# Performance work log

Hardware: AMD Instinct MI355X
Metric: run time of the kernel (lower is better)

Reference implementation:

```python
import jax, jax.numpy as jnp
import numpy as np

B, S, N = 64, 32, 128            # batch, seq_len, padded nodes per graph
DV, DW, DH = 512, 300, 1024      # dim_v, dim_word, dim_hidden
CLS, T_CTRL, L = 1024, 12, 4     # cls_fc_dim, controller steps, stack_len
NQ, NA, NE, NATTR, M = 100, 28, 16, 1000, 6  # vocabs, edge cats, attrs, num modules
# module order: 0 NoOp, 1 Find(push), 2 Transform, 3 Filter, 4 And, 5 Describe

def _valid_mat():
    m = np.zeros((L, M), dtype=np.float32)
    for s in range(L):
        m[s, 0] = 1.0
        m[s, 1] = 1.0 if s < L - 1 else 0.0
        m[s, 2] = 1.0 if s >= 1 else 0.0
        m[s, 3] = 1.0 if s >= 1 else 0.0
        m[s, 4] = 1.0 if s >= 2 else 0.0
        m[s, 5] = 1.0 if s >= 1 else 0.0
    return jnp.asarray(m)

VALID_MAT = _valid_mat()

def setup_inputs() -> dict:
    key = jax.random.key(0)
    ks = jax.random.split(key, 24)
    nrm = lambda k, sh, sc: jax.random.normal(k, sh, jnp.float32) * sc
    inp = {}
    inp['questions'] = jax.random.randint(ks[0], (B, S), 0, NQ)
    inp['questions_len'] = jax.random.randint(ks[1], (B,), 8, S + 1)
    inp['conn'] = (jax.random.uniform(ks[2], (B, N, N)) < 0.2).astype(jnp.float32)
    inp['cat_mat'] = jax.random.randint(ks[3], (B, N, N), 0, NE)
    inp['v_idx'] = jax.random.randint(ks[4], (B, N), 0, NATTR)
    inp['attr_emb'] = nrm(ks[5], (NATTR, DV), 1.0 / np.sqrt(DV))
    inp['edge_cat_vectors'] = nrm(ks[6], (NE, DV), 1.0 / np.sqrt(DV))
    inp['enc_emb'] = nrm(ks[7], (NQ, DW), 1.0 / np.sqrt(DW))
    inp['Wx'] = nrm(ks[8], (DW, 4 * DH), 1.0 / np.sqrt(DW))
    inp['Wh'] = nrm(ks[9], (DH, 4 * DH), 1.0 / np.sqrt(DH))
    inp['b_lstm'] = jnp.zeros((4 * DH,), jnp.float32)
    inp['W_cq'] = nrm(ks[10], (2 * DH, DH), 1.0 / np.sqrt(2 * DH))
    inp['b_cq'] = jnp.zeros((DH,), jnp.float32)
    inp['W_mod'] = nrm(ks[11], (DH, M), 1.0 / np.sqrt(DH))
    inp['W_att'] = nrm(ks[12], (DH, DH), 1.0 / np.sqrt(DH))
    inp['W_q'] = nrm(ks[13], (DH, DV), np.sqrt(2.0 / DH))
    inp['b_q'] = jnp.zeros((DV,), jnp.float32)
    inp['W_find'] = nrm(ks[14], (DV, DV), 1.0 / np.sqrt(DV))
    inp['W_desc'] = nrm(ks[15], (DV, DV), 1.0 / np.sqrt(DV))
    inp['W_cls1'] = nrm(ks[16], (DV + DH, CLS), np.sqrt(2.0 / (DV + DH)))
    inp['b_cls1'] = jnp.zeros((CLS,), jnp.float32)
    inp['W_cls2'] = nrm(ks[17], (CLS, NA), np.sqrt(2.0 / CLS))
    inp['b_cls2'] = jnp.zeros((NA,), jnp.float32)
    return inp

def _read(st, p):
    return jnp.einsum('bnl,bl->bn', st, p)

def _write(st, p, a):
    pe = p[:, None, :]
    return a[:, :, None] * pe + st * (1.0 - pe)

def _ptr_fw(p):
    q = jnp.concatenate([jnp.zeros_like(p[:, :1]), p[:, :-1]], axis=1)
    return q.at[:, -1].add(p[:, -1])

def _ptr_bw(p):
    q = jnp.concatenate([p[:, 1:], jnp.zeros_like(p[:, :1])], axis=1)
    return q.at[:, 0].add(p[:, 0])

def reference(questions, questions_len, conn, cat_mat, v_idx, attr_emb,
              edge_cat_vectors, enc_emb, Wx, Wh, b_lstm, W_cq, b_cq, W_mod,
              W_att, W_q, b_q, W_find, W_desc, W_cls1, b_cls1, W_cls2, b_cls2):
    # ---- question encoder: embedding + LSTM over time-major sequence ----
    emb = enc_emb[questions].transpose(1, 0, 2)  # [S,B,DW]

    def lstm_step(carry, x):
        h, c = carry
        g = x @ Wx + h @ Wh + b_lstm
        i, f, gg, o = jnp.split(g, 4, axis=-1)
        c = jax.nn.sigmoid(f) * c + jax.nn.sigmoid(i) * jnp.tanh(gg)
        h = jax.nn.sigmoid(o) * jnp.tanh(c)
        return (h, c), h

    init = (jnp.zeros((B, DH), jnp.float32), jnp.zeros((B, DH), jnp.float32))
    _, outs = jax.lax.scan(lstm_step, init, emb)            # [S,B,DH]
    outs_b = outs.transpose(1, 0, 2)                         # [B,S,DH]
    q_hidden = outs_b[jnp.arange(B), questions_len - 1]      # last valid state

    mask = jnp.arange(S)[:, None] < questions_len[None, :]   # [S,B]
    feat = attr_emb[v_idx]                                   # [B,N,DV]
    bidx = jnp.arange(B)[:, None, None]

    att_stack = jnp.zeros((B, N, L), jnp.float32)
    stack_ptr = jnp.zeros((B, L), jnp.float32).at[:, 0].set(1.0)
    mem = jnp.zeros((B, DV), jnp.float32)
    c_ctrl = jnp.zeros((B, DH), jnp.float32)
    inv_sqrt_dv = 1.0 / np.sqrt(DV)

    for t in range(T_CTRL):
        # ---- controller step: module distribution + textual attention ----
        cq = jnp.tanh(jnp.concatenate([c_ctrl, q_hidden], axis=1) @ W_cq + b_cq)
        module_prob = jax.nn.softmax(cq @ W_mod, axis=-1)     # [B,M]
        al = jnp.einsum('sbh,bh->sb', outs, cq @ W_att)
        cv = jax.nn.softmax(jnp.where(mask, al, -1e9), axis=0)
        c_ctrl = jnp.einsum('sb,sbh->bh', cv, outs)
        c_i = jax.nn.relu(c_ctrl @ W_q + b_q)                 # [B,DV]

        # ---- validity masking of module distribution ----
        validity = jnp.round(stack_ptr @ VALID_MAT)           # [B,M]
        mp = module_prob * validity
        s = jnp.sum(mp, axis=1, keepdims=True)
        mp = mp / jnp.where(s > 0, s, 1.0)

        # ---- run every module, soft-average by module prob ----
        a_find = jax.nn.sigmoid(jnp.einsum('bnd,bd->bn', feat @ W_find, c_i) * inv_sqrt_dv)
        a_in = _read(att_stack, stack_ptr)
        # Transform: edge-category-weighted message passing on graph
        we = jax.nn.softmax(c_i @ edge_cat_vectors.T, axis=-1)   # [B,NE]
        ew = we[bidx, cat_mat] * conn                            # [B,N,N]
        a_trans = jnp.minimum(jnp.einsum('bij,bj->bi', ew, a_in), 1.0)
        p_fw = _ptr_fw(stack_ptr)
        p_bw = _ptr_bw(stack_ptr)
        a_prev = _read(att_stack, p_bw)
        pooled = jnp.einsum('bn,bnd->bd', a_in, feat) / (jnp.sum(a_in, 1, keepdims=True) + 1e-6)
        res = [
            (att_stack, stack_ptr, mem),                                  # NoOp
            (_write(att_stack, p_fw, a_find), p_fw, mem),                 # Find (push)
            (_write(att_stack, stack_ptr, a_trans), stack_ptr, mem),      # Transform
            (_write(att_stack, stack_ptr, a_in * a_find), stack_ptr, mem),# Filter
            (_write(att_stack, p_bw, jnp.minimum(a_prev, a_in)), p_bw, mem),  # And (pop)
            (att_stack, p_bw, pooled @ W_desc),                           # Describe
        ]
        att_stack = jnp.einsum('bm,mbnl->bnl', mp, jnp.stack([r[0] for r in res]))
        stack_ptr = jnp.einsum('bm,mbl->bl', mp, jnp.stack([r[1] for r in res]))
        mem = jnp.einsum('bm,mbd->bd', mp, jnp.stack([r[2] for r in res]))

    final = jnp.concatenate([mem, q_hidden], axis=1)
    h1 = jax.nn.relu(final @ W_cls1 + b_cls1)
    logits = h1 @ W_cls2 + b_cls2
    return logits
```

## Files before the change

### kernel.cpp

```cpp
#include <hip/hip_runtime.h>
#include <math.h>

#define B 64
#define S 32
#define NN 128
#define DV 512
#define DW 300
#define DH 1024
#define CLS 1024
#define T_CTRL 12
#define LL 4
#define NA 28
#define NE 16
#define MM 6

__device__ __forceinline__ float sigmoidf_(float x) { return 1.0f / (1.0f + expf(-x)); }

template<bool TRANS, class AF, class WF>
__device__ __forceinline__ void gemm_core(int kbeg, int Kc, AF loadA, WF loadW, float* part, int Cld) {
  __shared__ float Ast[2][64 * 36];
  __shared__ float Ws[2][32 * 64];
  const int tid = threadIdx.x;
  const int j0 = blockIdx.x * 64;
  const int ntiles = Kc >> 5;
  const int rg = tid & 15, cg = tid >> 4;
  float4 av[2], wv[2];

  auto fetch = [&](int kt) {
    #pragma unroll
    for (int i2 = 0; i2 < 2; ++i2) {
      int idx = tid + i2 * 256;
      av[i2] = loadA(idx >> 3, kt + (idx & 7) * 4);
    }
    #pragma unroll
    for (int i2 = 0; i2 < 2; ++i2) {
      int idx = tid + i2 * 256;
      if (!TRANS) wv[i2] = loadW(kt + (idx >> 4), j0 + (idx & 15) * 4);
      else        wv[i2] = loadW(j0 + (idx >> 3), kt + (idx & 7) * 4);
    }
  };
  auto commit = [&](int buf) {
    #pragma unroll
    for (int i2 = 0; i2 < 2; ++i2) {
      int idx = tid + i2 * 256;
      *(float4*)&Ast[buf][(idx >> 3) * 36 + (idx & 7) * 4] = av[i2];
    }
    #pragma unroll
    for (int i2 = 0; i2 < 2; ++i2) {
      int idx = tid + i2 * 256;
      if (!TRANS) {
        *(float4*)&Ws[buf][(idx >> 4) * 64 + (idx & 15) * 4] = wv[i2];
      } else {
        int jloc = idx >> 3, k4 = (idx & 7) * 4;
        Ws[buf][(k4 + 0) * 64 + jloc] = wv[i2].x;
        Ws[buf][(k4 + 1) * 64 + jloc] = wv[i2].y;
        Ws[buf][(k4 + 2) * 64 + jloc] = wv[i2].z;
        Ws[buf][(k4 + 3) * 64 + jloc] = wv[i2].w;
      }
    }
  };

  float acc[4][4] = {};
  fetch(kbeg);
  commit(0);
  __syncthreads();
  for (int i = 0; i < ntiles; ++i) {
    if (i + 1 < ntiles) fetch(kbeg + (i + 1) * 32);
    const float* As = &Ast[i & 1][0];
    const float* Wp = &Ws[i & 1][0];
    #pragma unroll
    for (int kq = 0; kq < 8; ++kq) {
      float4 a0 = *(const float4*)&As[(rg     ) * 36 + kq * 4];
      float4 a1 = *(const float4*)&As[(rg + 16) * 36 + kq * 4];
      float4 a2 = *(const float4*)&As[(rg + 32) * 36 + kq * 4];
      float4 a3 = *(const float4*)&As[(rg + 48) * 36 + kq * 4];
      float4 w0 = *(const float4*)&Wp[(kq * 4 + 0) * 64 + cg * 4];
      float4 w1 = *(const float4*)&Wp[(kq * 4 + 1) * 64 + cg * 4];
      float4 w2 = *(const float4*)&Wp[(kq * 4 + 2) * 64 + cg * 4];
      float4 w3 = *(const float4*)&Wp[(kq * 4 + 3) * 64 + cg * 4];
      #define STEP(m, AV) \
        acc[m][0]=fmaf(AV.x,w0.x,acc[m][0]); acc[m][1]=fmaf(AV.x,w0.y,acc[m][1]); \
        acc[m][2]=fmaf(AV.x,w0.z,acc[m][2]); acc[m][3]=fmaf(AV.x,w0.w,acc[m][3]); \
        acc[m][0]=fmaf(AV.y,w1.x,acc[m][0]); acc[m][1]=fmaf(AV.y,w1.y,acc[m][1]); \
        acc[m][2]=fmaf(AV.y,w1.z,acc[m][2]); acc[m][3]=fmaf(AV.y,w1.w,acc[m][3]); \
        acc[m][0]=fmaf(AV.z,w2.x,acc[m][0]); acc[m][1]=fmaf(AV.z,w2.y,acc[m][1]); \
        acc[m][2]=fmaf(AV.z,w2.z,acc[m][2]); acc[m][3]=fmaf(AV.z,w2.w,acc[m][3]); \
        acc[m][0]=fmaf(AV.w,w3.x,acc[m][0]); acc[m][1]=fmaf(AV.w,w3.y,acc[m][1]); \
        acc[m][2]=fmaf(AV.w,w3.z,acc[m][2]); acc[m][3]=fmaf(AV.w,w3.w,acc[m][3]);
      STEP(0, a0) STEP(1, a1) STEP(2, a2) STEP(3, a3)
      #undef STEP
    }
    if (i + 1 < ntiles) { __syncthreads(); commit((i + 1) & 1); __syncthreads(); }
  }
  float* op = part + (size_t)blockIdx.y * 64 * Cld + j0 + cg * 4;
  #pragma unroll
  for (int m = 0; m < 4; ++m)
    *(float4*)&op[(size_t)(rg + 16 * m) * Cld] = make_float4(acc[m][0], acc[m][1], acc[m][2], acc[m][3]);
}

__global__ void init_kernel(float* c_lstm, float* c_ctrl, float* att_stack, float* mem, float* sptr) {
  int idx = blockIdx.x * 256 + threadIdx.x;
  if (idx < B * DH) { c_lstm[idx] = 0.f; c_ctrl[idx] = 0.f; }
  if (idx < B * NN * LL) att_stack[idx] = 0.f;
  if (idx < B * DV) mem[idx] = 0.f;
  if (idx < B * LL) sptr[idx] = ((idx & (LL - 1)) == 0) ? 1.f : 0.f;
}

__global__ void embq_kernel(const int* __restrict__ questions, const float* __restrict__ enc_emb,
                            float* __restrict__ embq) {
  int row = blockIdx.x;
  int t = row >> 6, b = row & 63;
  int qid = questions[b * S + t];
  int c = threadIdx.x;
  embq[(size_t)row * 320 + c] = (c < DW) ? enc_emb[(size_t)qid * DW + c] : 0.f;
}

__global__ __launch_bounds__(256) void xgemm_kernel(const float* __restrict__ embq,
                                                    const float* __restrict__ Wx,
                                                    float* __restrict__ X) {
  auto Al = [&](int r, int k) -> float4 {
    return *(const float4*)&embq[(size_t)(blockIdx.y * 64 + r) * 320 + k];
  };
  auto Wl = [&](int k, int j) -> float4 {
    if (k < 300) return *(const float4*)&Wx[(size_t)k * 4096 + j];
    return make_float4(0.f, 0.f, 0.f, 0.f);
  };
  gemm_core<false>(0, 320, Al, Wl, X, 4096);
}

__global__ __launch_bounds__(256) void lstm_gemm_kernel(const float* __restrict__ h_prev,
                                                        const float* __restrict__ Wh,
                                                        float* __restrict__ part) {
  auto Al = [&](int r, int k) -> float4 { return *(const float4*)&h_prev[(size_t)r * 1024 + k]; };
  auto Wl = [&](int k, int j) -> float4 { return *(const float4*)&Wh[(size_t)k * 4096 + j]; };
  gemm_core<false>(blockIdx.y * 256, 256, Al, Wl, part, 4096);
}

__global__ __launch_bounds__(256) void lstm_gate_kernel(const float* __restrict__ part, int SK,
                                                        const float* __restrict__ X, int t,
                                                        const float* __restrict__ b_lstm,
                                                        float* __restrict__ h_out, float* __restrict__ c_st) {
  int idx = blockIdx.x * 256 + threadIdx.x;
  int b = idx >> 10, j = idx & 1023;
  const float* xr = X + ((size_t)t * 64 + b) * 4096;
  float gi = xr[j], gf = xr[1024 + j], gg = xr[2048 + j], go = xr[3072 + j];
  const float* pb = part + (size_t)b * 4096;
  for (int c = 0; c < SK; ++c) {
    const float* p = pb + (size_t)c * 262144;
    gi += p[j]; gf += p[1024 + j]; gg += p[2048 + j]; go += p[3072 + j];
  }
  gi += b_lstm[j]; gf += b_lstm[1024 + j]; gg += b_lstm[2048 + j]; go += b_lstm[3072 + j];
  float c = sigmoidf_(gf) * c_st[idx] + sigmoidf_(gi) * tanhf(gg);
  h_out[idx] = sigmoidf_(go) * tanhf(c);
  c_st[idx] = c;
}

__global__ __launch_bounds__(256) void c1_kernel(const float* __restrict__ c_ctrl,
                                                 const float* __restrict__ outs, const int* __restrict__ qlen,
                                                 const float* __restrict__ W_cq, float* __restrict__ partA,
                                                 const float* __restrict__ partE, const float* __restrict__ mp,
                                                 float* __restrict__ mem, int do_epi) {
  if (blockIdx.x == 16) {
    if (!do_epi) return;
    int t0 = blockIdx.y * 256 + threadIdx.x;
    #pragma unroll
    for (int i = 0; i < 4; ++i) {
      int f4 = t0 + i * 2048;
      int b = f4 >> 7, j = (f4 & 127) * 4;
      const float* m = &mp[b * 6];
      float s04 = m[0] + m[1] + m[2] + m[3] + m[4];
      float4 s = make_float4(0.f, 0.f, 0.f, 0.f);
      for (int c = 0; c < 8; ++c) {
        float4 v = *(const float4*)&partE[(size_t)c * 32768 + b * 512 + j];
        s.x += v.x; s.y += v.y; s.z += v.z; s.w += v.w;
      }
      float4 o = *(const float4*)&mem[b * 512 + j];
      o.x = s04 * o.x + m[5] * s.x; o.y = s04 * o.y + m[5] * s.y;
      o.z = s04 * o.z + m[5] * s.z; o.w = s04 * o.w + m[5] * s.w;
      *(float4*)&mem[b * 512 + j] = o;
    }
    return;
  }
  auto Al = [&](int r, int k) -> float4 {
    if (k < 1024) return *(const float4*)&c_ctrl[r * 1024 + k];
    int tq = qlen[r] - 1;
    return *(const float4*)&outs[(size_t)tq * 65536 + r * 1024 + (k - 1024)];
  };
  auto Wl = [&](int k, int j) -> float4 { return *(const float4*)&W_cq[(size_t)k * 1024 + j]; };
  gemm_core<false>(blockIdx.y * 256, 256, Al, Wl, partA, 1024);
}

__global__ __launch_bounds__(256) void c2_kernel(const float* __restrict__ partA,
                                                 const float* __restrict__ b_cq,
                                                 const float* __restrict__ W_att,
                                                 const float* __restrict__ W_mod,
                                                 float* __restrict__ partB) {
  auto Al = [&](int r, int k) -> float4 {
    float4 s = *(const float4*)&b_cq[k];
    for (int c = 0; c < 8; ++c) {
      float4 v = *(const float4*)&partA[(size_t)c * 65536 + r * 1024 + k];
      s.x += v.x; s.y += v.y; s.z += v.z; s.w += v.w;
    }
    return make_float4(tanhf(s.x), tanhf(s.y), tanhf(s.z), tanhf(s.w));
  };
  auto Wl = [&](int k, int j) -> float4 {
    if (j < 1024) return *(const float4*)&W_att[(size_t)k * 1024 + j];
    float v[4];
    #pragma unroll
    for (int i = 0; i < 4; ++i) {
      int jj = j + i;
      v[i] = (jj < 1030) ? W_mod[(size_t)k * 6 + (jj - 1024)] : 0.f;
    }
    return make_float4(v[0], v[1], v[2], v[3]);
  };
  gemm_core<false>(blockIdx.y * 64, 64, Al, Wl, partB, 1088);
}

__global__ __launch_bounds__(256) void attn_kernel(const float* __restrict__ partB,
                                                   const float* __restrict__ outs,
                                                   const int* __restrict__ qlen,
                                                   float* __restrict__ c_ctrl) {
  int b = blockIdx.x >> 2, hq = blockIdx.x & 3;
  int tid = threadIdx.x;
  __shared__ float aw[DH];
  __shared__ float alv[S];
  __shared__ float cvs[S];
  {
    int c4 = tid * 4;
    float4 s = make_float4(0.f, 0.f, 0.f, 0.f);
    for (int c = 0; c < 16; ++c) {
      float4 v = *(const float4*)&partB[(size_t)c * 69632 + b * 1088 + c4];
      s.x += v.x; s.y += v.y; s.z += v.z; s.w += v.w;
    }
    *(float4*)&aw[c4] = s;
  }
  __syncthreads();
  {
    int wv = tid >> 6, lane = tid & 63;
    #pragma unroll
    for (int u = 0; u < 4; ++u) {
      int s2 = wv * 4 + u;
      const float4* orow = (const float4*)&outs[(size_t)s2 * 65536 + b * 1024];
      float pr = 0.f;
      #pragma unroll
      for (int q = 0; q < 4; ++q) {
        float4 f = orow[lane + 64 * q];
        float4 w = *(const float4*)&aw[(lane + 64 * q) * 4];
        pr += f.x * w.x + f.y * w.y + f.z * w.z + f.w * w.w;
      }
      #pragma unroll
      for (int off = 32; off > 0; off >>= 1) pr += __shfl_xor(pr, off);
      if (lane == 0) alv[s2] = pr;
    }
  }
  __syncthreads();
  if (tid < 64) {
    int len = qlen[b];
    float v = (tid < S && tid < len) ? alv[tid] : -1e9f;
    float mx = v;
    #pragma unroll
    for (int off = 32; off > 0; off >>= 1) mx = fmaxf(mx, __shfl_xor(mx, off));
    float e = (tid < S && tid < len) ? expf(v - mx) : 0.f;
    float sm = e;
    #pragma unroll
    for (int off = 32; off > 0; off >>= 1) sm += __shfl_xor(sm, off);
    if (tid < S) cvs[tid] = e / sm;
  }
  __syncthreads();
  {
    int h = hq * 256 + tid;
    float a = 0.f;
    #pragma unroll 8
    for (int s2 = 0; s2 < S; ++s2)
      a = fmaf(cvs[s2], outs[(size_t)s2 * 65536 + b * 1024 + h], a);
    c_ctrl[b * 1024 + h] = a;
  }
}

__global__ __launch_bounds__(256) void c4_kernel(const float* __restrict__ c_ctrl,
                                                 const float* __restrict__ W_q,
                                                 float* __restrict__ partC) {
  auto Al = [&](int r, int k) -> float4 { return *(const float4*)&c_ctrl[r * 1024 + k]; };
  auto Wl = [&](int k, int j) -> float4 { return *(const float4*)&W_q[(size_t)k * 512 + j]; };
  gemm_core<false>(blockIdx.y * 64, 64, Al, Wl, partC, 512);
}

__global__ __launch_bounds__(256) void c5_kernel(const float* __restrict__ partC,
                                                 const float* __restrict__ b_q,
                                                 const float* __restrict__ W_find,
                                                 const float* __restrict__ edge_cat,
                                                 float* __restrict__ partD) {
  auto Al = [&](int r, int k) -> float4 {
    float4 s = *(const float4*)&b_q[k];
    for (int c = 0; c < 16; ++c) {
      float4 v = *(const float4*)&partC[(size_t)c * 32768 + r * 512 + k];
      s.x += v.x; s.y += v.y; s.z += v.z; s.w += v.w;
    }
    return make_float4(fmaxf(s.x, 0.f), fmaxf(s.y, 0.f), fmaxf(s.z, 0.f), fmaxf(s.w, 0.f));
  };
  auto Wl = [&](int j, int k) -> float4 {
    if (j < 512) return *(const float4*)&W_find[(size_t)j * 512 + k];
    if (j < 528) return *(const float4*)&edge_cat[(size_t)(j - 512) * 512 + k];
    return make_float4(0.f, 0.f, 0.f, 0.f);
  };
  gemm_core<true>(blockIdx.y * 64, 64, Al, Wl, partD, 576);
}

__global__ __launch_bounds__(256) void prep_kernel(const float* __restrict__ partD,
                                                   const float* __restrict__ partB,
                                                   const float* __restrict__ sptr_in,
                                                   const float* __restrict__ att_stack,
                                                   float* __restrict__ uwe, float* __restrict__ we,
                                                   float* __restrict__ mp, float* __restrict__ spv,
                                                   float* __restrict__ ain, float* __restrict__ aw4,
                                                   float* __restrict__ asum) {
  int b = blockIdx.x, tid = threadIdx.x;
  __shared__ float lds[64];
  for (int col = tid; col < 528; col += 256) {
    float s = 0.f;
    for (int c = 0; c < 8; ++c) s += partD[(size_t)c * 36864 + b * 576 + col];
    uwe[b * 528 + col] = s;
    if (col >= 512) lds[col - 512] = s;
  }
  if (tid < MM) {
    float s = 0.f;
    for (int c = 0; c < 16; ++c) s += partB[(size_t)c * 69632 + b * 1088 + 1024 + tid];
    lds[16 + tid] = s;
  }
  __syncthreads();
  if (tid == 0) {
    float mx = lds[0];
    for (int e = 1; e < NE; ++e) mx = fmaxf(mx, lds[e]);
    float sm = 0.f, ex[NE];
    for (int e = 0; e < NE; ++e) { ex[e] = expf(lds[e] - mx); sm += ex[e]; }
    for (int e = 0; e < NE; ++e) we[b * NE + e] = ex[e] / sm;
    float mx2 = lds[16];
    for (int m = 1; m < MM; ++m) mx2 = fmaxf(mx2, lds[16 + m]);
    float e6[MM], sm2 = 0.f;
    for (int m = 0; m < MM; ++m) { e6[m] = expf(lds[16 + m] - mx2); sm2 += e6[m]; }
    float p0 = sptr_in[b * 4 + 0], p1 = sptr_in[b * 4 + 1];
    float p2 = sptr_in[b * 4 + 2], p3 = sptr_in[b * 4 + 3];
    float sp[12];
    sp[0] = p0; sp[1] = p1; sp[2] = p2; sp[3] = p3;
    sp[4] = 0.f;      sp[5] = p0; sp[6] = p1; sp[7] = p2 + p3;
    sp[8] = p0 + p1;  sp[9] = p2; sp[10] = p3; sp[11] = 0.f;
    for (int i = 0; i < 12; ++i) { spv[b * 12 + i] = sp[i]; lds[22 + i] = sp[i]; }
    float val[MM];
    val[0] = rintf(p0 + p1 + p2 + p3);
    val[1] = rintf(p0 + p1 + p2);
    val[2] = rintf(p1 + p2 + p3);
    val[3] = val[2];
    val[4] = rintf(p2 + p3);
    val[5] = val[2];
    float mpv[MM], ssum = 0.f;
    #pragma unroll
    for (int m = 0; m < MM; ++m) { mpv[m] = (e6[m] / sm2) * val[m]; ssum += mpv[m]; }
    float inv = (ssum > 0.f) ? 1.f / ssum : 1.f;
    #pragma unroll
    for (int m = 0; m < MM; ++m) mp[b * MM + m] = mpv[m] * inv;
  }
  __syncthreads();
  if (tid < 128) {
    float4 st = *(const float4*)&att_stack[(b * NN + tid) * LL];
    float ainv = st.x * lds[22] + st.y * lds[23] + st.z * lds[24] + st.w * lds[25];
    float ap   = st.x * lds[30] + st.y * lds[31] + st.z * lds[32] + st.w * lds[33];
    ain[b * NN + tid] = ainv;
    aw4[b * NN + tid] = fminf(ap, ainv);
    float t2 = ainv;
    #pragma unroll
    for (int off = 32; off > 0; off >>= 1) t2 += __shfl_xor(t2, off);
    if ((tid & 63) == 0) lds[40 + (tid >> 6)] = t2;
  }
  __syncthreads();
  if (tid == 0) asum[b] = lds[40] + lds[41] + 1e-6f;
}

__global__ __launch_bounds__(256) void stackf_kernel(const int* __restrict__ v_idx,
                                                     const float* __restrict__ attr_emb,
                                                     const float* __restrict__ uwe,
                                                     const float* __restrict__ we,
                                                     const int* __restrict__ cat_mat,
                                                     const float* __restrict__ conn,
                                                     const float* __restrict__ ain,
                                                     const float* __restrict__ asum,
                                                     float* __restrict__ afind,
                                                     float* __restrict__ atr,
                                                     float* __restrict__ pooled) {
  int job = blockIdx.x, tid = threadIdx.x;
  __shared__ float lds[192];
  if (job < 2048) {
    int gw = job * 4 + (tid >> 6);
    int b = gw >> 7, n = gw & 127, lane = tid & 63;
    int vid = v_idx[b * NN + n];
    const float4* fp = (const float4*)&attr_emb[(size_t)vid * DV];
    const float4* up = (const float4*)&uwe[(size_t)b * 528];
    float pr = 0.f;
    #pragma unroll
    for (int q = 0; q < 2; ++q) {
      float4 f = fp[lane + 64 * q], u = up[lane + 64 * q];
      pr += f.x * u.x + f.y * u.y + f.z * u.z + f.w * u.w;
    }
    #pragma unroll
    for (int off = 32; off > 0; off >>= 1) pr += __shfl_xor(pr, off);
    if (lane == 0) afind[b * NN + n] = sigmoidf_(pr * 0.04419417382415922f);
  } else if (job < 2560) {
    int j2 = job - 2048;
    int b = j2 >> 3, ig = j2 & 7;
    if (tid < 128) lds[tid] = ain[b * NN + tid];
    else if (tid < 144) lds[tid] = we[b * NE + tid - 128];
    __syncthreads();
    int i = ig * 16 + (tid >> 4);
    const int* crow = &cat_mat[((size_t)b * NN + i) * NN];
    const float* nrow = &conn[((size_t)b * NN + i) * NN];
    float a = 0.f;
    #pragma unroll
    for (int q = 0; q < 8; ++q) {
      int j = (tid & 15) + 16 * q;
      a = fmaf(lds[128 + crow[j]] * nrow[j], lds[j], a);
    }
    a += __shfl_xor(a, 1); a += __shfl_xor(a, 2); a += __shfl_xor(a, 4); a += __shfl_xor(a, 8);
    if ((tid & 15) == 0) atr[b * NN + i] = fminf(a, 1.f);
  } else {
    int j3 = job - 2560;
    int b = j3 >> 1, d = (j3 & 1) * 256 + tid;
    int* vidL = (int*)&lds[128];
    if (tid < 128) { lds[tid] = ain[b * NN + tid]; vidL[tid] = v_idx[b * NN + tid]; }
    __syncthreads();
    float a = 0.f;
    #pragma unroll 4
    for (int n = 0; n < NN; ++n)
      a = fmaf(lds[n], attr_emb[(size_t)vidL[n] * DV + d], a);
    pooled[b * DV + d] = a / asum[b];
  }
}

__global__ __launch_bounds__(256) void c7u_kernel(const float* __restrict__ pooled,
                                                  const float* __restrict__ W_desc,
                                                  float* __restrict__ partE,
                                                  const float* __restrict__ spv,
                                                  const float* __restrict__ mp,
                                                  const float* __restrict__ afind,
                                                  const float* __restrict__ ain,
                                                  const float* __restrict__ atr,
                                                  const float* __restrict__ aw4,
                                                  float* __restrict__ att_stack,
                                                  float* __restrict__ sptr) {
  int tid = threadIdx.x;
  if (blockIdx.y < 8) {
    auto Al = [&](int r, int k) -> float4 { return *(const float4*)&pooled[r * 512 + k]; };
    auto Wl = [&](int k, int j) -> float4 { return *(const float4*)&W_desc[(size_t)k * 512 + j]; };
    gemm_core<false>(blockIdx.y * 64, 64, Al, Wl, partE, 512);
    return;
  }
  int b = (blockIdx.y - 8) * 8 + blockIdx.x;
  __shared__ float sp[12], smp[MM];
  if (tid < 12) sp[tid] = spv[b * 12 + tid];
  else if (tid < 12 + MM) smp[tid - 12] = mp[b * MM + (tid - 12)];
  __syncthreads();
  #pragma unroll
  for (int i = 0; i < 2; ++i) {
    int e = tid + i * 256;
    int n = e >> 2, l = e & 3;
    float st = att_stack[(b * NN + n) * LL + l];
    float keep = smp[0] + smp[5] + smp[1] * (1.f - sp[4 + l]) + (smp[2] + smp[3]) * (1.f - sp[l])
               + smp[4] * (1.f - sp[8 + l]);
    float add = sp[4 + l] * smp[1] * afind[b * NN + n]
              + sp[l] * (smp[2] * atr[b * NN + n] + smp[3] * ain[b * NN + n] * afind[b * NN + n])
              + sp[8 + l] * smp[4] * aw4[b * NN + n];
    att_stack[(b * NN + n) * LL + l] = keep * st + add;
  }
  if (tid < LL)
    sptr[b * LL + tid] = (smp[0] + smp[2] + smp[3]) * sp[tid] + smp[1] * sp[4 + tid]
                       + (smp[4] + smp[5]) * sp[8 + tid];
}

__global__ __launch_bounds__(256) void cl1_kernel(const float* __restrict__ partE,
                                                  const float* __restrict__ mp,
                                                  const float* __restrict__ mem,
                                                  const float* __restrict__ outs,
                                                  const int* __restrict__ qlen,
                                                  const float* __restrict__ W_cls1,
                                                  float* __restrict__ partH) {
  auto Al = [&](int r, int k) -> float4 {
    if (k < 512) {
      float4 s = make_float4(0.f, 0.f, 0.f, 0.f);
      for (int c = 0; c < 8; ++c) {
        float4 v = *(const float4*)&partE[(size_t)c * 32768 + r * 512 + k];
        s.x += v.x; s.y += v.y; s.z += v.z; s.w += v.w;
      }
      const float* m = &mp[r * 6];
      float s04 = m[0] + m[1] + m[2] + m[3] + m[4];
      float4 o = *(const float4*)&mem[r * 512 + k];
      return make_float4(s04 * o.x + m[5] * s.x, s04 * o.y + m[5] * s.y,
                         s04 * o.z + m[5] * s.z, s04 * o.w + m[5] * s.w);
    }
    int tq = qlen[r] - 1;
    return *(const float4*)&outs[(size_t)tq * 65536 + r * 1024 + (k - 512)];
  };
  auto Wl = [&](int k, int j) -> float4 { return *(const float4*)&W_cls1[(size_t)k * 1024 + j]; };
  gemm_core<false>(blockIdx.y * 192, 192, Al, Wl, partH, 1024);
}

__global__ __launch_bounds__(256) void cl2_kernel(const float* __restrict__ partH,
                                                  const float* __restrict__ b_cls1,
                                                  const float* __restrict__ W_cls2,
                                                  float* __restrict__ partJ) {
  auto Al = [&](int r, int k) -> float4 {
    float4 s = *(const float4*)&b_cls1[k];
    for (int c = 0; c < 8; ++c) {
      float4 v = *(const float4*)&partH[(size_t)c * 65536 + r * 1024 + k];
      s.x += v.x; s.y += v.y; s.z += v.z; s.w += v.w;
    }
    return make_float4(fmaxf(s.x, 0.f), fmaxf(s.y, 0.f), fmaxf(s.z, 0.f), fmaxf(s.w, 0.f));
  };
  auto Wl = [&](int k, int j) -> float4 {
    float v[4];
    #pragma unroll
    for (int i = 0; i < 4; ++i) { int jj = j + i; v[i] = (jj < NA) ? W_cls2[(size_t)k * NA + jj] : 0.f; }
    return make_float4(v[0], v[1], v[2], v[3]);
  };
  gemm_core<false>(blockIdx.y * 128, 128, Al, Wl, partJ, 64);
}

__global__ void cl3_kernel(const float* __restrict__ partJ, const float* __restrict__ b_cls2,
                           float* __restrict__ logits) {
  int idx = blockIdx.x * 256 + threadIdx.x;
  if (idx >= B * NA) return;
  int r = idx / NA, j = idx - r * NA;
  float s = b_cls2[j];
  for (int c = 0; c < 8; ++c) s += partJ[(size_t)c * 4096 + r * 64 + j];
  logits[idx] = s;
}

extern "C" void kernel_launch(void* const* d_in, const int* in_sizes, int n_in,
                              void* d_out, int out_size, void* d_ws, size_t ws_size,
                              hipStream_t stream) {
  const int*   questions = (const int*)d_in[0];
  const int*   qlen      = (const int*)d_in[1];
  const float* conn      = (const float*)d_in[2];
  const int*   cat_mat   = (const int*)d_in[3];
  const int*   v_idx     = (const int*)d_in[4];
  const float* attr_emb  = (const float*)d_in[5];
  const float* edge_cat  = (const float*)d_in[6];
  const float* enc_emb   = (const float*)d_in[7];
  const float* Wx        = (const float*)d_in[8];
  const float* Wh        = (const float*)d_in[9];
  const float* b_lstm    = (const float*)d_in[10];
  const float* W_cq      = (const float*)d_in[11];
  const float* b_cq      = (const float*)d_in[12];
  const float* W_mod     = (const float*)d_in[13];
  const float* W_att     = (const float*)d_in[14];
  const float* W_q       = (const float*)d_in[15];
  const float* b_q       = (const float*)d_in[16];
  const float* W_find    = (const float*)d_in[17];
  const float* W_desc    = (const float*)d_in[18];
  const float* W_cls1    = (const float*)d_in[19];
  const float* b_cls1    = (const float*)d_in[20];
  const float* W_cls2    = (const float*)d_in[21];
  const float* b_cls2    = (const float*)d_in[22];
  float* logits = (float*)d_out;

  float* w = (float*)d_ws;
  size_t off = 0;
  float* outs      = w + off; off += (size_t)S * B * DH;
  float* embq      = w + off; off += (size_t)S * B * 320;
  float* X         = w + off; off += (size_t)S * B * 4096;
  float* share     = w + off; off += 2457600;
  float* partE     = w + off; off += 262144;
  float* partH     = w + off; off += 524288;
  float* partJ     = w + off; off += 32768;
  float* c_ctrl    = w + off; off += B * DH;
  float* c_lstm    = w + off; off += B * DH;
  float* uwe_buf   = w + off; off += B * 528;
  float* we_buf    = w + off; off += B * NE;
  float* mp_buf    = w + off; off += B * MM;
  float* spv_buf   = w + off; off += B * 12;
  float* ain_buf   = w + off; off += B * NN;
  float* aw4_buf   = w + off; off += B * NN;
  float* afind_buf = w + off; off += B * NN;
  float* atr_buf   = w + off; off += B * NN;
  float* asum_buf  = w + off; off += B;
  float* att_stack = w + off; off += B * NN * LL;
  float* sptr_buf  = w + off; off += B * LL;
  float* mem       = w + off; off += B * DV;
  float* pooled    = w + off; off += B * DV;

  float* partLSTM = share;
  float* partA = share;
  float* partB = share + 524288;
  float* partC = share + 1638400;
  float* partD = share + 2162688;

  init_kernel<<<256, 256, 0, stream>>>(c_lstm, c_ctrl, att_stack, mem, sptr_buf);
  embq_kernel<<<S * B, 320, 0, stream>>>(questions, enc_emb, embq);
  xgemm_kernel<<<dim3(64, 32), 256, 0, stream>>>(embq, Wx, X);

  for (int t = 0; t < S; ++t) {
    if (t > 0) {
      lstm_gemm_kernel<<<dim3(64, 4), 256, 0, stream>>>(outs + (size_t)(t - 1) * B * DH, Wh, partLSTM);
      lstm_gate_kernel<<<(B * DH) / 256, 256, 0, stream>>>(partLSTM, 4, X, t, b_lstm,
                                                           outs + (size_t)t * B * DH, c_lstm);
    } else {
      lstm_gate_kernel<<<(B * DH) / 256, 256, 0, stream>>>(partLSTM, 0, X, 0, b_lstm,
                                                           outs, c_lstm);
    }
  }

  for (int it = 0; it < T_CTRL; ++it) {
    c1_kernel<<<dim3(17, 8), 256, 0, stream>>>(c_ctrl, outs, qlen, W_cq, partA,
                                               partE, mp_buf, mem, it > 0 ? 1 : 0);
    c2_kernel<<<dim3(17, 16), 256, 0, stream>>>(partA, b_cq, W_att, W_mod, partB);
    attn_kernel<<<256, 256, 0, stream>>>(partB, outs, qlen, c_ctrl);
    c4_kernel<<<dim3(8, 16), 256, 0, stream>>>(c_ctrl, W_q, partC);
    c5_kernel<<<dim3(9, 8), 256, 0, stream>>>(partC, b_q, W_find, edge_cat, partD);
    prep_kernel<<<64, 256, 0, stream>>>(partD, partB, sptr_buf, att_stack,
                                        uwe_buf, we_buf, mp_buf, spv_buf, ain_buf, aw4_buf, asum_buf);
    stackf_kernel<<<2688, 256, 0, stream>>>(v_idx, attr_emb, uwe_buf, we_buf, cat_mat, conn,
                                            ain_buf, asum_buf, afind_buf, atr_buf, pooled);
    c7u_kernel<<<dim3(8, 16), 256, 0, stream>>>(pooled, W_desc, partE, spv_buf, mp_buf,
                                                afind_buf, ain_buf, atr_buf, aw4_buf,
                                                att_stack, sptr_buf);
  }

  cl1_kernel<<<dim3(16, 8), 256, 0, stream>>>(partE, mp_buf, mem, outs, qlen, W_cls1, partH);
  cl2_kernel<<<dim3(1, 8), 256, 0, stream>>>(partH, b_cls1, W_cls2, partJ);
  cl3_kernel<<<7, 256, 0, stream>>>(partJ, b_cls2, logits);
}
```

Baseline: 1.502 ms.

## Precompute attr_emb@W_find, overlap X projection with LSTM steps, widen K-split

Reassociates the find score so that attr_emb·W_find is computed once up front (F2), and each controller step only needs relu(c·W_q+b) dotted with F2 rows. This drops the per-iteration c5 GEMM, and the edge-category dot products move into prep_kernel as warp reductions. The input projection X is no longer computed for all timesteps up front. Instead, the x-GEMM for step t+1 runs inside the same launch as the recurrent GEMM, double-buffered in a small Xbuf. The recurrent GEMM split-K is also widened from 4 to 8 chunks to fill more CUs, which adds more partial sums for the gate kernel to read.

```diff
diff --git a/kernel.cpp b/kernel.cpp
--- a/kernel.cpp
+++ b/kernel.cpp
@@ -17,7 +17,8 @@
 __device__ __forceinline__ float sigmoidf_(float x) { return 1.0f / (1.0f + expf(-x)); }
 
 template<bool TRANS, class AF, class WF>
-__device__ __forceinline__ void gemm_core(int kbeg, int Kc, AF loadA, WF loadW, float* part, int Cld) {
+__device__ __forceinline__ void gemm_core(int kbeg, int Kc, AF loadA, WF loadW,
+                                          float* part, int Cld, int orow) {
   __shared__ float Ast[2][64 * 36];
   __shared__ float Ws[2][32 * 64];
   const int tid = threadIdx.x;
@@ -92,7 +93,7 @@
     }
     if (i + 1 < ntiles) { __syncthreads(); commit((i + 1) & 1); __syncthreads(); }
   }
-  float* op = part + (size_t)blockIdx.y * 64 * Cld + j0 + cg * 4;
+  float* op = part + (size_t)orow * 64 * Cld + j0 + cg * 4;
   #pragma unroll
   for (int m = 0; m < 4; ++m)
     *(float4*)&op[(size_t)(rg + 16 * m) * Cld] = make_float4(acc[m][0], acc[m][1], acc[m][2], acc[m][3]);
@@ -115,35 +116,69 @@
   embq[(size_t)row * 320 + c] = (c < DW) ? enc_emb[(size_t)qid * DW + c] : 0.f;
 }
 
-__global__ __launch_bounds__(256) void xgemm_kernel(const float* __restrict__ embq,
-                                                    const float* __restrict__ Wx,
-                                                    float* __restrict__ X) {
+__global__ __launch_bounds__(256) void xpre_kernel(const float* __restrict__ embq,
+                                                   const float* __restrict__ Wx,
+                                                   float* __restrict__ Xbuf) {
+  int t = blockIdx.y, ch = blockIdx.z;
   auto Al = [&](int r, int k) -> float4 {
-    return *(const float4*)&embq[(size_t)(blockIdx.y * 64 + r) * 320 + k];
+    return *(const float4*)&embq[(size_t)(t * 64 + r) * 320 + k];
   };
   auto Wl = [&](int k, int j) -> float4 {
     if (k < 300) return *(const float4*)&Wx[(size_t)k * 4096 + j];
     return make_float4(0.f, 0.f, 0.f, 0.f);
   };
-  gemm_core<false>(0, 320, Al, Wl, X, 4096);
+  gemm_core<false>(ch * 160, 160, Al, Wl, Xbuf + (size_t)t * 524288 + (size_t)ch * 262144, 4096, 0);
+}
+
+__global__ __launch_bounds__(256) void f2_kernel(const float* __restrict__ attr_emb,
+                                                 const float* __restrict__ W_find,
+                                                 float* __restrict__ F2) {
+  auto Al = [&](int r, int k) -> float4 {
+    int gr = blockIdx.y * 64 + r;
+    if (gr > 999) gr = 999;
+    return *(const float4*)&attr_emb[(size_t)gr * 512 + k];
+  };
+  auto Wl = [&](int k, int j) -> float4 { return *(const float4*)&W_find[(size_t)k * 512 + j]; };
+  gemm_core<false>(0, 512, Al, Wl, F2, 512, blockIdx.y);
 }
 
 __global__ __launch_bounds__(256) void lstm_gemm_kernel(const float* __restrict__ h_prev,
                                                         const float* __restrict__ Wh,
-                                                        float* __restrict__ part) {
-  auto Al = [&](int r, int k) -> float4 { return *(const float4*)&h_prev[(size_t)r * 1024 + k]; };
-  auto Wl = [&](int k, int j) -> float4 { return *(const float4*)&Wh[(size_t)k * 4096 + j]; };
-  gemm_core<false>(blockIdx.y * 256, 256, Al, Wl, part, 4096);
+                                                        float* __restrict__ part,
+                                                        const float* __restrict__ embq,
+                                                        const float* __restrict__ Wx,
+                                                        float* __restrict__ Xbuf, int t) {
+  if (blockIdx.y < 8) {
+    auto Al = [&](int r, int k) -> float4 { return *(const float4*)&h_prev[(size_t)r * 1024 + k]; };
+    auto Wl = [&](int k, int j) -> float4 { return *(const float4*)&Wh[(size_t)k * 4096 + j]; };
+    gemm_core<false>(blockIdx.y * 128, 128, Al, Wl, part, 4096, blockIdx.y);
+  } else {
+    if (t == 31) return;
+    int ch = blockIdx.y - 8;
+    auto Al = [&](int r, int k) -> float4 {
+      return *(const float4*)&embq[(size_t)((t + 1) * 64 + r) * 320 + k];
+    };
+    auto Wl = [&](int k, int j) -> float4 {
+      if (k < 300) return *(const float4*)&Wx[(size_t)k * 4096 + j];
+      return make_float4(0.f, 0.f, 0.f, 0.f);
+    };
+    gemm_core<false>(ch * 160, 160, Al, Wl,
+                     Xbuf + (size_t)((t + 1) & 1) * 524288 + (size_t)ch * 262144, 4096, 0);
+  }
 }
 
 __global__ __launch_bounds__(256) void lstm_gate_kernel(const float* __restrict__ part, int SK,
-                                                        const float* __restrict__ X, int t,
+                                                        const float* __restrict__ px,
                                                         const float* __restrict__ b_lstm,
                                                         float* __restrict__ h_out, float* __restrict__ c_st) {
   int idx = blockIdx.x * 256 + threadIdx.x;
   int b = idx >> 10, j = idx & 1023;
-  const float* xr = X + ((size_t)t * 64 + b) * 4096;
-  float gi = xr[j], gf = xr[1024 + j], gg = xr[2048 + j], go = xr[3072 + j];
+  const float* x0 = px + (size_t)b * 4096;
+  const float* x1 = px + 262144 + (size_t)b * 4096;
+  float gi = x0[j] + x1[j];
+  float gf = x0[1024 + j] + x1[1024 + j];
+  float gg = x0[2048 + j] + x1[2048 + j];
+  float go = x0[3072 + j] + x1[3072 + j];
   const float* pb = part + (size_t)b * 4096;
   for (int c = 0; c < SK; ++c) {
     const float* p = pb + (size_t)c * 262144;
@@ -187,7 +222,7 @@
     return *(const float4*)&outs[(size_t)tq * 65536 + r * 1024 + (k - 1024)];
   };
   auto Wl = [&](int k, int j) -> float4 { return *(const float4*)&W_cq[(size_t)k * 1024 + j]; };
-  gemm_core<false>(blockIdx.y * 256, 256, Al, Wl, partA, 1024);
+  gemm_core<false>(blockIdx.y * 256, 256, Al, Wl, partA, 1024, blockIdx.y);
 }
 
 __global__ __launch_bounds__(256) void c2_kernel(const float* __restrict__ partA,
@@ -213,7 +248,7 @@
     }
     return make_float4(v[0], v[1], v[2], v[3]);
   };
-  gemm_core<false>(blockIdx.y * 64, 64, Al, Wl, partB, 1088);
+  gemm_core<false>(blockIdx.y * 64, 64, Al, Wl, partB, 1088, blockIdx.y);
 }
 
 __global__ __launch_bounds__(256) void attn_kernel(const float* __restrict__ partB,
@@ -282,50 +317,46 @@
                                                  float* __restrict__ partC) {
   auto Al = [&](int r, int k) -> float4 { return *(const float4*)&c_ctrl[r * 1024 + k]; };
   auto Wl = [&](int k, int j) -> float4 { return *(const float4*)&W_q[(size_t)k * 512 + j]; };
-  gemm_core<false>(blockIdx.y * 64, 64, Al, Wl, partC, 512);
-}
-
-__global__ __launch_bounds__(256) void c5_kernel(const float* __restrict__ partC,
-                                                 const float* __restrict__ b_q,
-                                                 const float* __restrict__ W_find,
-                                                 const float* __restrict__ edge_cat,
-                                                 float* __restrict__ partD) {
-  auto Al = [&](int r, int k) -> float4 {
-    float4 s = *(const float4*)&b_q[k];
-    for (int c = 0; c < 16; ++c) {
-      float4 v = *(const float4*)&partC[(size_t)c * 32768 + r * 512 + k];
-      s.x += v.x; s.y += v.y; s.z += v.z; s.w += v.w;
-    }
-    return make_float4(fmaxf(s.x, 0.f), fmaxf(s.y, 0.f), fmaxf(s.z, 0.f), fmaxf(s.w, 0.f));
-  };
-  auto Wl = [&](int j, int k) -> float4 {
-    if (j < 512) return *(const float4*)&W_find[(size_t)j * 512 + k];
-    if (j < 528) return *(const float4*)&edge_cat[(size_t)(j - 512) * 512 + k];
-    return make_float4(0.f, 0.f, 0.f, 0.f);
-  };
-  gemm_core<true>(blockIdx.y * 64, 64, Al, Wl, partD, 576);
-}
-
-__global__ __launch_bounds__(256) void prep_kernel(const float* __restrict__ partD,
+  gemm_core<false>(blockIdx.y * 64, 64, Al, Wl, partC, 512, blockIdx.y);
+}
+
+__global__ __launch_bounds__(256) void prep_kernel(const float* __restrict__ partC,
                                                    const float* __restrict__ partB,
+                                                   const float* __restrict__ b_q,
+                                                   const float* __restrict__ edge_cat,
                                                    const float* __restrict__ sptr_in,
                                                    const float* __restrict__ att_stack,
-                                                   float* __restrict__ uwe, float* __restrict__ we,
+                                                   float* __restrict__ c_i, float* __restrict__ we,
                                                    float* __restrict__ mp, float* __restrict__ spv,
                                                    float* __restrict__ ain, float* __restrict__ aw4,
                                                    float* __restrict__ asum) {
   int b = blockIdx.x, tid = threadIdx.x;
+  __shared__ float ci[512];
   __shared__ float lds[64];
-  for (int col = tid; col < 528; col += 256) {
-    float s = 0.f;
-    for (int c = 0; c < 8; ++c) s += partD[(size_t)c * 36864 + b * 576 + col];
-    uwe[b * 528 + col] = s;
-    if (col >= 512) lds[col - 512] = s;
+  for (int col = tid; col < 512; col += 256) {
+    float s = b_q[col];
+    for (int c = 0; c < 16; ++c) s += partC[(size_t)c * 32768 + b * 512 + col];
+    s = fmaxf(s, 0.f);
+    ci[col] = s;
+    c_i[b * 512 + col] = s;
   }
   if (tid < MM) {
     float s = 0.f;
     for (int c = 0; c < 16; ++c) s += partB[(size_t)c * 69632 + b * 1088 + 1024 + tid];
     lds[16 + tid] = s;
+  }
+  __syncthreads();
+  {
+    int wv = tid >> 6, lane = tid & 63;
+    for (int e = wv; e < NE; e += 4) {
+      const float* er = &edge_cat[(size_t)e * 512];
+      float p = 0.f;
+      #pragma unroll
+      for (int q = 0; q < 8; ++q) p = fmaf(ci[lane + 64 * q], er[lane + 64 * q], p);
+      #pragma unroll
+      for (int off = 32; off > 0; off >>= 1) p += __shfl_xor(p, off);
+      if (lane == 0) lds[e] = p;
+    }
   }
   __syncthreads();
   if (tid == 0) {
@@ -377,7 +408,8 @@
 
 __global__ __launch_bounds__(256) void stackf_kernel(const int* __restrict__ v_idx,
                                                      const float* __restrict__ attr_emb,
-                                                     const float* __restrict__ uwe,
+                                                     const float* __restrict__ F2,
+                                                     const float* __restrict__ c_i,
                                                      const float* __restrict__ we,
                                                      const int* __restrict__ cat_mat,
                                                      const float* __restrict__ conn,
@@ -392,8 +424,8 @@
     int gw = job * 4 + (tid >> 6);
     int b = gw >> 7, n = gw & 127, lane = tid & 63;
     int vid = v_idx[b * NN + n];
-    const float4* fp = (const float4*)&attr_emb[(size_t)vid * DV];
-    const float4* up = (const float4*)&uwe[(size_t)b * 528];
+    const float4* fp = (const float4*)&F2[(size_t)vid * DV];
+    const float4* up = (const float4*)&c_i[(size_t)b * DV];
     float pr = 0.f;
     #pragma unroll
     for (int q = 0; q < 2; ++q) {
@@ -449,7 +481,7 @@
   if (blockIdx.y < 8) {
     auto Al = [&](int r, int k) -> float4 { return *(const float4*)&pooled[r * 512 + k]; };
     auto Wl = [&](int k, int j) -> float4 { return *(const float4*)&W_desc[(size_t)k * 512 + j]; };
-    gemm_core<false>(blockIdx.y * 64, 64, Al, Wl, partE, 512);
+    gemm_core<false>(blockIdx.y * 64, 64, Al, Wl, partE, 512, blockIdx.y);
     return;
   }
   int b = (blockIdx.y - 8) * 8 + blockIdx.x;
@@ -498,7 +530,7 @@
     return *(const float4*)&outs[(size_t)tq * 65536 + r * 1024 + (k - 512)];
   };
   auto Wl = [&](int k, int j) -> float4 { return *(const float4*)&W_cls1[(size_t)k * 1024 + j]; };
-  gemm_core<false>(blockIdx.y * 192, 192, Al, Wl, partH, 1024);
+  gemm_core<false>(blockIdx.y * 192, 192, Al, Wl, partH, 1024, blockIdx.y);
 }
 
 __global__ __launch_bounds__(256) void cl2_kernel(const float* __restrict__ partH,
@@ -519,7 +551,7 @@
     for (int i = 0; i < 4; ++i) { int jj = j + i; v[i] = (jj < NA) ? W_cls2[(size_t)k * NA + jj] : 0.f; }
     return make_float4(v[0], v[1], v[2], v[3]);
   };
-  gemm_core<false>(blockIdx.y * 128, 128, Al, Wl, partJ, 64);
+  gemm_core<false>(blockIdx.y * 128, 128, Al, Wl, partJ, 64, blockIdx.y);
 }
 
 __global__ void cl3_kernel(const float* __restrict__ partJ, const float* __restrict__ b_cls2,
@@ -564,14 +596,15 @@
   size_t off = 0;
   float* outs      = w + off; off += (size_t)S * B * DH;
   float* embq      = w + off; off += (size_t)S * B * 320;
-  float* X         = w + off; off += (size_t)S * B * 4096;
+  float* Xbuf      = w + off; off += 2 * 2 * 262144;
+  float* F2        = w + off; off += 1024 * 512;
   float* share     = w + off; off += 2457600;
   float* partE     = w + off; off += 262144;
   float* partH     = w + off; off += 524288;
   float* partJ     = w + off; off += 32768;
   float* c_ctrl    = w + off; off += B * DH;
   float* c_lstm    = w + off; off += B * DH;
-  float* uwe_buf   = w + off; off += B * 528;
+  float* ci_buf    = w + off; off += B * DV;
   float* we_buf    = w + off; off += B * NE;
   float* mp_buf    = w + off; off += B * MM;
   float* spv_buf   = w + off; off += B * 12;
@@ -589,21 +622,18 @@
   float* partA = share;
   float* partB = share + 524288;
   float* partC = share + 1638400;
-  float* partD = share + 2162688;
 
   init_kernel<<<256, 256, 0, stream>>>(c_lstm, c_ctrl, att_stack, mem, sptr_buf);
   embq_kernel<<<S * B, 320, 0, stream>>>(questions, enc_emb, embq);
-  xgemm_kernel<<<dim3(64, 32), 256, 0, stream>>>(embq, Wx, X);
-
-  for (int t = 0; t < S; ++t) {
-    if (t > 0) {
-      lstm_gemm_kernel<<<dim3(64, 4), 256, 0, stream>>>(outs + (size_t)(t - 1) * B * DH, Wh, partLSTM);
-      lstm_gate_kernel<<<(B * DH) / 256, 256, 0, stream>>>(partLSTM, 4, X, t, b_lstm,
-                                                           outs + (size_t)t * B * DH, c_lstm);
-    } else {
-      lstm_gate_kernel<<<(B * DH) / 256, 256, 0, stream>>>(partLSTM, 0, X, 0, b_lstm,
-                                                           outs, c_lstm);
-    }
+  xpre_kernel<<<dim3(64, 2, 2), 256, 0, stream>>>(embq, Wx, Xbuf);
+  f2_kernel<<<dim3(8, 16), 256, 0, stream>>>(attr_emb, W_find, F2);
+
+  lstm_gate_kernel<<<(B * DH) / 256, 256, 0, stream>>>(partLSTM, 0, Xbuf, b_lstm, outs, c_lstm);
+  for (int t = 1; t < S; ++t) {
+    lstm_gemm_kernel<<<dim3(64, 10), 256, 0, stream>>>(outs + (size_t)(t - 1) * B * DH, Wh,
+                                                       partLSTM, embq, Wx, Xbuf, t);
+    lstm_gate_kernel<<<(B * DH) / 256, 256, 0, stream>>>(partLSTM, 8, Xbuf + (size_t)(t & 1) * 524288,
+                                                         b_lstm, outs + (size_t)t * B * DH, c_lstm);
   }
 
   for (int it = 0; it < T_CTRL; ++it) {
@@ -612,10 +642,9 @@
     c2_kernel<<<dim3(17, 16), 256, 0, stream>>>(partA, b_cq, W_att, W_mod, partB);
     attn_kernel<<<256, 256, 0, stream>>>(partB, outs, qlen, c_ctrl);
     c4_kernel<<<dim3(8, 16), 256, 0, stream>>>(c_ctrl, W_q, partC);
-    c5_kernel<<<dim3(9, 8), 256, 0, stream>>>(partC, b_q, W_find, edge_cat, partD);
-    prep_kernel<<<64, 256, 0, stream>>>(partD, partB, sptr_buf, att_stack,
-                                        uwe_buf, we_buf, mp_buf, spv_buf, ain_buf, aw4_buf, asum_buf);
-    stackf_kernel<<<2688, 256, 0, stream>>>(v_idx, attr_emb, uwe_buf, we_buf, cat_mat, conn,
+    prep_kernel<<<64, 256, 0, stream>>>(partC, partB, b_q, edge_cat, sptr_buf, att_stack,
+                                        ci_buf, we_buf, mp_buf, spv_buf, ain_buf, aw4_buf, asum_buf);
+    stackf_kernel<<<2688, 256, 0, stream>>>(v_idx, attr_emb, F2, ci_buf, we_buf, cat_mat, conn,
                                             ain_buf, asum_buf, afind_buf, atr_buf, pooled);
     c7u_kernel<<<dim3(8, 16), 256, 0, stream>>>(pooled, W_desc, partE, spv_buf, mp_buf,
                                                 afind_buf, ain_buf, atr_buf, aw4_buf,
```

Result: slower. 1.575 ms (+4.8%).
